# Performance work log

Measured on AMD Instinct MI355X. Metric: run time of the kernel, lower is better.

## Reference

```python
import jax, jax.numpy as jnp
import numpy as np

B, IN, H, D, C, K = 4096, 128, 256, 32, 8, 256
HS = D // 2  # structure_filter hidden (latent_dim > 2)
EPS = 1e-6
MAX_NORM = 0.99


def _gelu(t):
    return jax.nn.gelu(t, approximate=False)  # torch nn.GELU default = exact erf


def _project_to_ball(z):
    norm = jnp.maximum(jnp.linalg.norm(z, axis=-1, keepdims=True), EPS)
    scale = jnp.minimum(MAX_NORM / norm, 1.0)
    return z * scale


def _hyperbolic_distance(xp, yp):
    # Poincare-ball distance: arccosh(1 + 2*|x-y|^2 / ((1-|x|^2)(1-|y|^2)))
    sq = jnp.sum((xp - yp) ** 2, axis=-1)
    xn = jnp.sum(xp * xp, axis=-1)
    yn = jnp.sum(yp * yp, axis=-1)
    denom = jnp.maximum((1.0 - xn) * (1.0 - yn), EPS)
    arg = jnp.maximum(1.0 + 2.0 * sq / denom, 1.0 + EPS)
    return jnp.arccosh(arg)


def setup_inputs() -> dict:
    key = jax.random.key(0)
    ks = jax.random.split(key, 14)
    n = lambda k, shape, s: (jax.random.normal(k, shape, dtype=jnp.float32) * s)
    centers = jax.random.normal(ks[7], (C, D), dtype=jnp.float32)
    centers = centers / jnp.maximum(jnp.linalg.norm(centers, axis=-1, keepdims=True), EPS)
    return {
        "x": jax.random.normal(ks[0], (B, IN), dtype=jnp.float32),
        "W1": n(ks[1], (IN, H), 0.05), "b1": jnp.zeros((H,), jnp.float32),
        "W2": n(ks[2], (H, H), 0.05), "b2": jnp.zeros((H,), jnp.float32),
        "Wv": n(ks[3], (H, D), 0.05), "bv": jnp.zeros((D,), jnp.float32),
        "centers": centers,
        "codebook": n(ks[8], (C, K, D), 0.02),
        "Ws1": n(ks[9], (D, HS), 0.1), "bs1": jnp.zeros((HS,), jnp.float32),
        "Ws2": n(ks[10], (HS, D), 0.1), "bs2": jnp.zeros((D,), jnp.float32),
    }


def reference(x, W1, b1, W2, b2, Wv, bv, centers, codebook, Ws1, bs1, Ws2, bs2):
    sg = jax.lax.stop_gradient
    feats = _gelu(_gelu(x @ W1 + b1) @ W2 + b2)          # [B,H]
    v = feats @ Wv + bv                                   # [B,D]
    scores = (v @ centers.T) / jnp.sqrt(jnp.asarray(D, v.dtype))
    router = jax.nn.softmax(scores, axis=-1)              # [B,C]
    K_chart = jnp.argmax(router, axis=1)                  # [B]
    c_bar = router @ centers                              # [B,D]
    v_local = v - c_bar                                   # [B,D]
    diff = v_local[:, None, None, :] - codebook[None]     # [B,C,K,D]
    dist = jnp.sum(diff * diff, axis=-1)                  # [B,C,K]
    indices = jnp.argmin(dist, axis=-1)                   # [B,C]
    z_q_all = codebook[jnp.arange(C)[None, :], indices]   # [B,C,D]
    v_bc = jnp.broadcast_to(v_local[:, None, :], z_q_all.shape)
    v_proj = _project_to_ball(v_bc)
    w_det = sg(router)
    d_cb = _hyperbolic_distance(z_q_all, sg(v_proj))      # [B,C]
    codebook_loss = jnp.sum(jnp.mean(d_cb ** 2 * w_det, axis=0))
    d_cm = _hyperbolic_distance(sg(z_q_all), v_proj)
    commitment = jnp.sum(jnp.mean(d_cm ** 2 * w_det, axis=0))
    vq_loss = codebook_loss + 0.25 * commitment
    z_q_blended = jnp.sum(z_q_all * router[..., None], axis=1)  # [B,D]
    K_code = jnp.take_along_axis(indices, K_chart[:, None], axis=1)[:, 0]
    delta = v_local[:, None, :] - sg(z_q_all)             # [B,C,D]
    z_n_all = _gelu(delta @ Ws1 + bs1) @ Ws2 + bs2        # [B,C,D]
    z_n = jnp.sum(z_n_all * router[..., None], axis=1)    # [B,D]
    z_tex = (v_local - sg(z_q_blended)) - z_n
    z_q_st = v_local + sg(z_q_blended - v_local)
    z_geo = c_bar + z_q_st + z_n
    return (K_chart, K_code, z_n, z_tex, router, z_geo, vq_loss, indices, z_n_all, c_bar, v_local)
```

## Files before the change

### kernel.cpp

```cpp
#include <hip/hip_runtime.h>
#include <math.h>

#define NB 4096
#define NIN 128
#define NH 256
#define ND 32
#define NC 8
#define NK 256
#define NHS 16

#define OFF_KCHART 0
#define OFF_KCODE  4096
#define OFF_ZN     8192
#define OFF_ZTEX   (OFF_ZN + 4096*32)
#define OFF_ROUTER (OFF_ZTEX + 4096*32)
#define OFF_ZGEO   (OFF_ROUTER + 4096*8)
#define OFF_LOSS   (OFF_ZGEO + 4096*32)
#define OFF_IND    (OFF_LOSS + 1)
#define OFF_ZNALL  (OFF_IND + 4096*8)
#define OFF_CBAR   (OFF_ZNALL + 4096*8*32)
#define OFF_VLOC   (OFF_CBAR + 4096*32)

__device__ __forceinline__ float gelu_exact(float x) {
    return x * (erff(x / 1.41421356237309504f) + 1.0f) * 0.5f;
}

template<int K>
__global__ __launch_bounds__(256)
void gemm_bias_gelu(const float* __restrict__ A, const float* __restrict__ W,
                    const float* __restrict__ bias, float* __restrict__ out) {
    const int N = 256;
    __shared__ float sB[2][32][68];
    const int t  = threadIdx.x;
    const int n0 = blockIdx.x * 64;
    const int r0 = blockIdx.y * 64;
    const int ty = t >> 4, tx = t & 15;
    const int bk = t >> 4, bc = t & 15;

    float4 bias4 = *(const float4*)(bias + n0 + tx * 4);

    float4 pb0 = *(const float4*)(W + bk * N + n0 + bc * 4);
    float4 pb1 = *(const float4*)(W + (bk + 16) * N + n0 + bc * 4);

    const float* Ab0 = A + (r0 + ty * 4 + 0) * K;
    const float* Ab1 = A + (r0 + ty * 4 + 1) * K;
    const float* Ab2 = A + (r0 + ty * 4 + 2) * K;
    const float* Ab3 = A + (r0 + ty * 4 + 3) * K;
    float ac[4][4], an[4][4];
    {
        float4 c0 = *(const float4*)(Ab0 + 0), c1 = *(const float4*)(Ab1 + 0);
        float4 c2 = *(const float4*)(Ab2 + 0), c3 = *(const float4*)(Ab3 + 0);
        ac[0][0]=c0.x; ac[0][1]=c0.y; ac[0][2]=c0.z; ac[0][3]=c0.w;
        ac[1][0]=c1.x; ac[1][1]=c1.y; ac[1][2]=c1.z; ac[1][3]=c1.w;
        ac[2][0]=c2.x; ac[2][1]=c2.y; ac[2][2]=c2.z; ac[2][3]=c2.w;
        ac[3][0]=c3.x; ac[3][1]=c3.y; ac[3][2]=c3.z; ac[3][3]=c3.w;
        float4 n0v = *(const float4*)(Ab0 + 4), n1v = *(const float4*)(Ab1 + 4);
        float4 n2v = *(const float4*)(Ab2 + 4), n3v = *(const float4*)(Ab3 + 4);
        an[0][0]=n0v.x; an[0][1]=n0v.y; an[0][2]=n0v.z; an[0][3]=n0v.w;
        an[1][0]=n1v.x; an[1][1]=n1v.y; an[1][2]=n1v.z; an[1][3]=n1v.w;
        an[2][0]=n2v.x; an[2][1]=n2v.y; an[2][2]=n2v.z; an[2][3]=n2v.w;
        an[3][0]=n3v.x; an[3][1]=n3v.y; an[3][2]=n3v.z; an[3][3]=n3v.w;
    }

    float acc[4][4];
    #pragma unroll
    for (int i = 0; i < 4; i++)
        #pragma unroll
        for (int j = 0; j < 4; j++) acc[i][j] = 0.f;

    int buf = 0;
    for (int kk = 0; kk < K; kk += 32) {
        *(float4*)(&sB[buf][bk][bc*4])    = pb0;
        *(float4*)(&sB[buf][bk+16][bc*4]) = pb1;
        __syncthreads();
        if (kk + 32 < K) {
            pb0 = *(const float4*)(W + (kk + 32 + bk) * N + n0 + bc * 4);
            pb1 = *(const float4*)(W + (kk + 32 + bk + 16) * N + n0 + bc * 4);
        }
        #pragma unroll
        for (int c = 0; c < 8; c++) {
            int knext = kk + (c + 2) * 4;
            if (knext > K - 4) knext = K - 4;
            float4 p0 = *(const float4*)(Ab0 + knext);
            float4 p1 = *(const float4*)(Ab1 + knext);
            float4 p2 = *(const float4*)(Ab2 + knext);
            float4 p3 = *(const float4*)(Ab3 + knext);
            #pragma unroll
            for (int u = 0; u < 4; u++) {
                float4 bv = *(const float4*)(&sB[buf][c * 4 + u][tx * 4]);
                float bb[4] = {bv.x, bv.y, bv.z, bv.w};
                #pragma unroll
                for (int j = 0; j < 4; j++) {
                    acc[0][j] = fmaf(ac[0][u], bb[j], acc[0][j]);
                    acc[1][j] = fmaf(ac[1][u], bb[j], acc[1][j]);
                    acc[2][j] = fmaf(ac[2][u], bb[j], acc[2][j]);
                    acc[3][j] = fmaf(ac[3][u], bb[j], acc[3][j]);
                }
            }
            #pragma unroll
            for (int u = 0; u < 4; u++) {
                ac[0][u] = an[0][u]; ac[1][u] = an[1][u];
                ac[2][u] = an[2][u]; ac[3][u] = an[3][u];
            }
            an[0][0]=p0.x; an[0][1]=p0.y; an[0][2]=p0.z; an[0][3]=p0.w;
            an[1][0]=p1.x; an[1][1]=p1.y; an[1][2]=p1.z; an[1][3]=p1.w;
            an[2][0]=p2.x; an[2][1]=p2.y; an[2][2]=p2.z; an[2][3]=p2.w;
            an[3][0]=p3.x; an[3][1]=p3.y; an[3][2]=p3.z; an[3][3]=p3.w;
        }
        buf ^= 1;
    }
    float bb4[4] = {bias4.x, bias4.y, bias4.z, bias4.w};
    #pragma unroll
    for (int i = 0; i < 4; i++) {
        int row = r0 + ty * 4 + i;
        float4 o;
        float* op = (float*)&o;
        #pragma unroll
        for (int j = 0; j < 4; j++) op[j] = gelu_exact(acc[i][j] + bb4[j]);
        *(float4*)(out + row * N + n0 + tx * 4) = o;
    }
}

__global__ __launch_bounds__(256)
void router_kernel(const float* __restrict__ feats, const float* __restrict__ Wv,
                   const float* __restrict__ bv, const float* __restrict__ centers,
                   float* __restrict__ out, float* __restrict__ vloc_ws) {
    __shared__ float sWvT[ND][260];
    __shared__ float sCent[NC * ND];
    __shared__ float sV[16][ND + 1];
    __shared__ float sRout[16][NC];
    const int t = threadIdx.x;
    {
        #pragma unroll
        for (int q = 0; q < 8; q++) {
            int id = t + q * 256;
            int k = id >> 3, c4 = (id & 7) * 4;
            float4 w = ((const float4*)Wv)[id];
            sWvT[c4 + 0][k] = w.x;
            sWvT[c4 + 1][k] = w.y;
            sWvT[c4 + 2][k] = w.z;
            sWvT[c4 + 3][k] = w.w;
        }
        if (t < 64) ((float4*)sCent)[t] = ((const float4*)centers)[t];
    }
    __syncthreads();
    const int r = t >> 4, cp = t & 15;
    const int row = blockIdx.x * 16 + r;
    float a0 = bv[cp], a1 = bv[cp + 16];
    const float4* f4 = (const float4*)(feats + row * NH);
    for (int k4 = 0; k4 < NH / 4; k4++) {
        float4 f = f4[k4];
        float4 w0 = *(const float4*)(&sWvT[cp][k4 * 4]);
        float4 w1 = *(const float4*)(&sWvT[cp + 16][k4 * 4]);
        a0 = fmaf(f.x, w0.x, a0); a1 = fmaf(f.x, w1.x, a1);
        a0 = fmaf(f.y, w0.y, a0); a1 = fmaf(f.y, w1.y, a1);
        a0 = fmaf(f.z, w0.z, a0); a1 = fmaf(f.z, w1.z, a1);
        a0 = fmaf(f.w, w0.w, a0); a1 = fmaf(f.w, w1.w, a1);
    }
    sV[r][cp] = a0; sV[r][cp + 16] = a1;
    __syncthreads();
    if (t < 16) {
        const int rr = t, grow = blockIdx.x * 16 + rr;
        float sc[NC];
        float m = -3.4e38f; int kmax = 0;
        #pragma unroll
        for (int c = 0; c < NC; c++) {
            float acc = 0.f;
            #pragma unroll
            for (int k = 0; k < ND; k++) acc = fmaf(sV[rr][k], sCent[c * ND + k], acc);
            acc = acc / 5.65685424949238f;
            sc[c] = acc;
            if (acc > m) { m = acc; kmax = c; }
        }
        float s = 0.f;
        #pragma unroll
        for (int c = 0; c < NC; c++) { float e = expf(sc[c] - m); sc[c] = e; s += e; }
        float inv = 1.f / s;
        #pragma unroll
        for (int c = 0; c < NC; c++) {
            float rv = sc[c] * inv;
            sRout[rr][c] = rv;
            out[OFF_ROUTER + grow * NC + c] = rv;
        }
        out[OFF_KCHART + grow] = (float)kmax;
    }
    __syncthreads();
    #pragma unroll
    for (int j = 0; j < 2; j++) {
        int col = cp + j * 16;
        float cb = 0.f;
        #pragma unroll
        for (int c = 0; c < NC; c++) cb = fmaf(sRout[r][c], sCent[c * ND + col], cb);
        float vl = sV[r][col] - cb;
        out[OFF_CBAR + row * ND + col] = cb;
        out[OFF_VLOC + row * ND + col] = vl;
        vloc_ws[row * ND + col] = vl;
    }
}

__global__ __launch_bounds__(256)
void vq_chart(const float* __restrict__ codebook, const float* __restrict__ vloc_ws,
              const float* __restrict__ Ws1, const float* __restrict__ bs1,
              const float* __restrict__ Ws2, const float* __restrict__ bs2,
              float* __restrict__ out, float* __restrict__ loss_partial) {
    __shared__ float sCB[NK][36];
    __shared__ float sV[64][36];
    __shared__ float sBest[8][64];
    __shared__ int   sBidx[8][64];
    __shared__ int   sSel[64];
    __shared__ float sRoutv[64];
    __shared__ float sPscale[64];
    __shared__ float sLossArr[64];
    __shared__ float sWs1[ND][17];
    __shared__ float sWs2[NHS][33];
    __shared__ float sbs1[NHS], sbs2v[ND];
    const int t = threadIdx.x;
    const int c = blockIdx.x & 7;
    const int row0 = (blockIdx.x >> 3) * 64;

    {
        const float4* src = (const float4*)(codebook + c * NK * ND);
        #pragma unroll
        for (int q = 0; q < 8; q++) {
            int id = t + q * 256;
            int code = id >> 3, kq = (id & 7) * 4;
            *(float4*)(&sCB[code][kq]) = src[id];
        }
        #pragma unroll
        for (int q = 0; q < 2; q++) {
            int id = t + q * 256;
            int rr = id >> 3, kq = (id & 7) * 4;
            *(float4*)(&sV[rr][kq]) = ((const float4*)(vloc_ws + row0 * ND))[id];
        }
    }
    if (t < 128) {
        float4 w = ((const float4*)Ws1)[t];
        int k = t >> 2, o = (t & 3) * 4;
        sWs1[k][o] = w.x; sWs1[k][o+1] = w.y; sWs1[k][o+2] = w.z; sWs1[k][o+3] = w.w;
    } else {
        int u = t - 128;
        float4 w = ((const float4*)Ws2)[u];
        int k = u >> 3, o = (u & 7) * 4;
        sWs2[k][o] = w.x; sWs2[k][o+1] = w.y; sWs2[k][o+2] = w.z; sWs2[k][o+3] = w.w;
    }
    if (t < NHS) sbs1[t] = bs1[t];
    else if (t < NHS + ND) sbs2v[t - NHS] = bs2[t - NHS];
    if (t < 64) sRoutv[t] = out[OFF_ROUTER + (row0 + t) * NC + c];
    __syncthreads();

    const int r = t & 31, g = t >> 5;
    float vl0[ND], vl1[ND];
    #pragma unroll
    for (int q = 0; q < 8; q++) {
        float4 a = *(const float4*)(&sV[r][q * 4]);
        vl0[q*4] = a.x; vl0[q*4+1] = a.y; vl0[q*4+2] = a.z; vl0[q*4+3] = a.w;
        float4 b = *(const float4*)(&sV[r + 32][q * 4]);
        vl1[q*4] = b.x; vl1[q*4+1] = b.y; vl1[q*4+2] = b.z; vl1[q*4+3] = b.w;
    }
    float best0 = 3.4e38f, best1 = 3.4e38f;
    int bi0 = 0, bi1 = 0;
    for (int j = 0; j < 32; j++) {
        const int code = g * 32 + j;
        float dot0 = 0.f, dot1 = 0.f, en2 = 0.f;
        #pragma unroll
        for (int q = 0; q < 8; q++) {
            float4 e = *(const float4*)(&sCB[code][q * 4]);
            en2  = fmaf(e.x, e.x, en2);
            dot0 = fmaf(vl0[q*4+0], e.x, dot0); dot1 = fmaf(vl1[q*4+0], e.x, dot1);
            en2  = fmaf(e.y, e.y, en2);
            dot0 = fmaf(vl0[q*4+1], e.y, dot0); dot1 = fmaf(vl1[q*4+1], e.y, dot1);
            en2  = fmaf(e.z, e.z, en2);
            dot0 = fmaf(vl0[q*4+2], e.z, dot0); dot1 = fmaf(vl1[q*4+2], e.z, dot1);
            en2  = fmaf(e.w, e.w, en2);
            dot0 = fmaf(vl0[q*4+3], e.w, dot0); dot1 = fmaf(vl1[q*4+3], e.w, dot1);
        }
        float d0 = en2 - 2.f * dot0;
        float d1 = en2 - 2.f * dot1;
        if (d0 < best0) { best0 = d0; bi0 = code; }
        if (d1 < best1) { best1 = d1; bi1 = code; }
    }
    sBest[g][r] = best0;      sBidx[g][r] = bi0;
    sBest[g][r + 32] = best1; sBidx[g][r + 32] = bi1;
    __syncthreads();
    if (t < 64) {
        float bb = sBest[0][t]; int ii = sBidx[0][t];
        #pragma unroll
        for (int gg = 1; gg < 8; gg++) {
            float v = sBest[gg][t];
            if (v < bb) { bb = v; ii = sBidx[gg][t]; }
        }
        sSel[t] = ii;
        out[OFF_IND + (row0 + t) * NC + c] = (float)ii;
        float vn2 = 0.f;
        #pragma unroll
        for (int k = 0; k < ND; k++) { float v = sV[t][k]; vn2 = fmaf(v, v, vn2); }
        float norm = fmaxf(sqrtf(vn2), 1e-6f);
        sPscale[t] = fminf(0.99f / norm, 1.0f);
    }
    __syncthreads();

    const int i = t & 15, r16 = t >> 4;
    const float b1r = sbs1[i];
    const float bo0 = sbs2v[2*i], bo1 = sbs2v[2*i+1];
    #pragma unroll
    for (int pass = 0; pass < 4; pass++) {
        const int lrow = pass * 16 + r16;
        const int grow = row0 + lrow;
        const int sel = sSel[lrow];
        const float rc = sRoutv[lrow];
        const float ps = sPscale[lrow];
        float acc1 = b1r;
        #pragma unroll
        for (int k = 0; k < ND; k++) {
            float dlt = sV[lrow][k] - sCB[sel][k];
            acc1 = fmaf(dlt, sWs1[k][i], acc1);
        }
        float h = gelu_exact(acc1);
        float a0 = bo0, a1 = bo1;
        #pragma unroll
        for (int k = 0; k < NHS; k++) {
            float s1k = __shfl(h, k, 16);
            a0 = fmaf(s1k, sWs2[k][2*i],   a0);
            a1 = fmaf(s1k, sWs2[k][2*i+1], a1);
        }
        out[OFF_ZNALL + (grow * NC + c) * ND + 2*i]     = a0;
        out[OFF_ZNALL + (grow * NC + c) * ND + 2*i + 1] = a1;
        const float e0 = sCB[sel][2*i], e1 = sCB[sel][2*i+1];
        float yp0 = sV[lrow][2*i] * ps, yp1 = sV[lrow][2*i+1] * ps;
        float d0 = e0 - yp0, d1 = e1 - yp1;
        float sq = fmaf(d0, d0, d1 * d1);
        float xn = fmaf(e0, e0, e1 * e1);
        float yn = fmaf(yp0, yp0, yp1 * yp1);
        #pragma unroll
        for (int m = 1; m < 16; m <<= 1) {
            sq += __shfl_xor(sq, m, 16);
            xn += __shfl_xor(xn, m, 16);
            yn += __shfl_xor(yn, m, 16);
        }
        if (i == 0) {
            float denom = fmaxf((1.f - xn) * (1.f - yn), 1e-6f);
            float arg = fmaxf(1.f + 2.f * sq / denom, 1.f + 1e-6f);
            float dd = acoshf(arg);
            sLossArr[lrow] = dd * dd * rc;
        }
    }
    __syncthreads();
    if (t < 64) {
        float v = sLossArr[t];
        #pragma unroll
        for (int off = 32; off > 0; off >>= 1) v += __shfl_down(v, off, 64);
        if (t == 0) loss_partial[blockIdx.x] = v;
    }
}

__global__ __launch_bounds__(256)
void finalize2_kernel(const float* __restrict__ codebook, const float* __restrict__ vloc_ws,
                      float* __restrict__ out, const float* __restrict__ partials) {
    const int gid = blockIdx.x * 256 + threadIdx.x;
    const int row = gid >> 4;
    const int cp = gid & 15;
    float rout[NC]; int ind[NC];
    #pragma unroll
    for (int cc = 0; cc < NC; cc++) {
        rout[cc] = out[OFF_ROUTER + row * NC + cc];
        ind[cc]  = (int)out[OFF_IND + row * NC + cc];
    }
    float zn0 = 0.f, zn1 = 0.f, zq0 = 0.f, zq1 = 0.f;
    #pragma unroll
    for (int cc = 0; cc < NC; cc++) {
        const float rcc = rout[cc];
        zn0 = fmaf(out[OFF_ZNALL + (row * NC + cc) * ND + 2*cp],     rcc, zn0);
        zn1 = fmaf(out[OFF_ZNALL + (row * NC + cc) * ND + 2*cp + 1], rcc, zn1);
        const float* e = codebook + (cc * NK + ind[cc]) * ND + 2*cp;
        zq0 = fmaf(e[0], rcc, zq0);
        zq1 = fmaf(e[1], rcc, zq1);
    }
    const float v0 = vloc_ws[row * ND + 2*cp], v1 = vloc_ws[row * ND + 2*cp + 1];
    const float cb0 = out[OFF_CBAR + row * ND + 2*cp];
    const float cb1 = out[OFF_CBAR + row * ND + 2*cp + 1];
    out[OFF_ZN   + row * ND + 2*cp]     = zn0;
    out[OFF_ZN   + row * ND + 2*cp + 1] = zn1;
    out[OFF_ZTEX + row * ND + 2*cp]     = v0 - zq0 - zn0;
    out[OFF_ZTEX + row * ND + 2*cp + 1] = v1 - zq1 - zn1;
    out[OFF_ZGEO + row * ND + 2*cp]     = cb0 + zq0 + zn0;
    out[OFF_ZGEO + row * ND + 2*cp + 1] = cb1 + zq1 + zn1;
    if (cp == 0) {
        int kc = (int)out[OFF_KCHART + row];
        out[OFF_KCODE + row] = out[OFF_IND + row * NC + kc];
    }
    if (blockIdx.x == 0) {
        __shared__ float sTmp[4];
        const int t = threadIdx.x;
        float v = partials[t] + partials[t + 256];
        #pragma unroll
        for (int off = 32; off > 0; off >>= 1) v += __shfl_down(v, off, 64);
        if ((t & 63) == 0) sTmp[t >> 6] = v;
        __syncthreads();
        if (t == 0) out[OFF_LOSS] = 1.25f * (sTmp[0] + sTmp[1] + sTmp[2] + sTmp[3]) / 4096.f;
    }
}

extern "C" void kernel_launch(void* const* d_in, const int* in_sizes, int n_in,
                              void* d_out, int out_size, void* d_ws, size_t ws_size,
                              hipStream_t stream) {
    const float* x        = (const float*)d_in[0];
    const float* W1       = (const float*)d_in[1];
    const float* b1       = (const float*)d_in[2];
    const float* W2       = (const float*)d_in[3];
    const float* b2       = (const float*)d_in[4];
    const float* Wv       = (const float*)d_in[5];
    const float* bv       = (const float*)d_in[6];
    const float* centers  = (const float*)d_in[7];
    const float* codebook = (const float*)d_in[8];
    const float* Ws1      = (const float*)d_in[9];
    const float* bs1      = (const float*)d_in[10];
    const float* Ws2      = (const float*)d_in[11];
    const float* bs2      = (const float*)d_in[12];
    float* out = (float*)d_out;
    float* ws  = (float*)d_ws;

    float* h1       = ws;
    float* feats    = ws + 4096 * 256;
    float* vloc     = ws + 2 * 4096 * 256;
    float* partials = ws + 2 * 4096 * 256 + 4096 * 32;

    gemm_bias_gelu<128><<<dim3(4, 64), dim3(256), 0, stream>>>(x, W1, b1, h1);
    gemm_bias_gelu<256><<<dim3(4, 64), dim3(256), 0, stream>>>(h1, W2, b2, feats);
    router_kernel<<<dim3(256), dim3(256), 0, stream>>>(feats, Wv, bv, centers, out, vloc);
    vq_chart<<<dim3(512), dim3(256), 0, stream>>>(codebook, vloc, Ws1, bs1, Ws2, bs2, out, partials);
    finalize2_kernel<<<dim3(256), dim3(256), 0, stream>>>(codebook, vloc, out, partials);
}
```

Baseline: 69.60 us.

## Halve per-block row tiles to double grid sizes and precompute codebook norms

The two GEMM kernels now give each thread 2 rows instead of 4, so the row tile per block drops from 64 to 32 and the grid doubles to 512 blocks. The router kernel handles 8 rows per block with one output column per thread, and spreads the center scores over 64 threads. Finalize uses one column per thread with twice the blocks. The VQ kernel computes codebook squared norms once into shared memory instead of inside the distance loop. More blocks should fill the 256 CUs better, at the cost of less register reuse per thread in the GEMMs and more redundant weight and codebook staging per block.

```diff
diff --git a/kernel.cpp b/kernel.cpp
--- a/kernel.cpp
+++ b/kernel.cpp
@@ -33,7 +33,7 @@
     __shared__ float sB[2][32][68];
     const int t  = threadIdx.x;
     const int n0 = blockIdx.x * 64;
-    const int r0 = blockIdx.y * 64;
+    const int r0 = blockIdx.y * 32;
     const int ty = t >> 4, tx = t & 15;
     const int bk = t >> 4, bc = t & 15;
 
@@ -42,29 +42,21 @@
     float4 pb0 = *(const float4*)(W + bk * N + n0 + bc * 4);
     float4 pb1 = *(const float4*)(W + (bk + 16) * N + n0 + bc * 4);
 
-    const float* Ab0 = A + (r0 + ty * 4 + 0) * K;
-    const float* Ab1 = A + (r0 + ty * 4 + 1) * K;
-    const float* Ab2 = A + (r0 + ty * 4 + 2) * K;
-    const float* Ab3 = A + (r0 + ty * 4 + 3) * K;
-    float ac[4][4], an[4][4];
+    const float* Ab0 = A + (r0 + ty * 2 + 0) * K;
+    const float* Ab1 = A + (r0 + ty * 2 + 1) * K;
+    float ac[2][4], an[2][4];
     {
         float4 c0 = *(const float4*)(Ab0 + 0), c1 = *(const float4*)(Ab1 + 0);
-        float4 c2 = *(const float4*)(Ab2 + 0), c3 = *(const float4*)(Ab3 + 0);
         ac[0][0]=c0.x; ac[0][1]=c0.y; ac[0][2]=c0.z; ac[0][3]=c0.w;
         ac[1][0]=c1.x; ac[1][1]=c1.y; ac[1][2]=c1.z; ac[1][3]=c1.w;
-        ac[2][0]=c2.x; ac[2][1]=c2.y; ac[2][2]=c2.z; ac[2][3]=c2.w;
-        ac[3][0]=c3.x; ac[3][1]=c3.y; ac[3][2]=c3.z; ac[3][3]=c3.w;
-        float4 n0v = *(const float4*)(Ab0 + 4), n1v = *(const float4*)(Ab1 + 4);
-        float4 n2v = *(const float4*)(Ab2 + 4), n3v = *(const float4*)(Ab3 + 4);
-        an[0][0]=n0v.x; an[0][1]=n0v.y; an[0][2]=n0v.z; an[0][3]=n0v.w;
-        an[1][0]=n1v.x; an[1][1]=n1v.y; an[1][2]=n1v.z; an[1][3]=n1v.w;
-        an[2][0]=n2v.x; an[2][1]=n2v.y; an[2][2]=n2v.z; an[2][3]=n2v.w;
-        an[3][0]=n3v.x; an[3][1]=n3v.y; an[3][2]=n3v.z; an[3][3]=n3v.w;
-    }
-
-    float acc[4][4];
-    #pragma unroll
-    for (int i = 0; i < 4; i++)
+        float4 d0 = *(const float4*)(Ab0 + 4), d1 = *(const float4*)(Ab1 + 4);
+        an[0][0]=d0.x; an[0][1]=d0.y; an[0][2]=d0.z; an[0][3]=d0.w;
+        an[1][0]=d1.x; an[1][1]=d1.y; an[1][2]=d1.z; an[1][3]=d1.w;
+    }
+
+    float acc[2][4];
+    #pragma unroll
+    for (int i = 0; i < 2; i++)
         #pragma unroll
         for (int j = 0; j < 4; j++) acc[i][j] = 0.f;
 
@@ -83,8 +75,6 @@
             if (knext > K - 4) knext = K - 4;
             float4 p0 = *(const float4*)(Ab0 + knext);
             float4 p1 = *(const float4*)(Ab1 + knext);
-            float4 p2 = *(const float4*)(Ab2 + knext);
-            float4 p3 = *(const float4*)(Ab3 + knext);
             #pragma unroll
             for (int u = 0; u < 4; u++) {
                 float4 bv = *(const float4*)(&sB[buf][c * 4 + u][tx * 4]);
@@ -93,26 +83,19 @@
                 for (int j = 0; j < 4; j++) {
                     acc[0][j] = fmaf(ac[0][u], bb[j], acc[0][j]);
                     acc[1][j] = fmaf(ac[1][u], bb[j], acc[1][j]);
-                    acc[2][j] = fmaf(ac[2][u], bb[j], acc[2][j]);
-                    acc[3][j] = fmaf(ac[3][u], bb[j], acc[3][j]);
                 }
             }
             #pragma unroll
-            for (int u = 0; u < 4; u++) {
-                ac[0][u] = an[0][u]; ac[1][u] = an[1][u];
-                ac[2][u] = an[2][u]; ac[3][u] = an[3][u];
-            }
+            for (int u = 0; u < 4; u++) { ac[0][u] = an[0][u]; ac[1][u] = an[1][u]; }
             an[0][0]=p0.x; an[0][1]=p0.y; an[0][2]=p0.z; an[0][3]=p0.w;
             an[1][0]=p1.x; an[1][1]=p1.y; an[1][2]=p1.z; an[1][3]=p1.w;
-            an[2][0]=p2.x; an[2][1]=p2.y; an[2][2]=p2.z; an[2][3]=p2.w;
-            an[3][0]=p3.x; an[3][1]=p3.y; an[3][2]=p3.z; an[3][3]=p3.w;
         }
         buf ^= 1;
     }
     float bb4[4] = {bias4.x, bias4.y, bias4.z, bias4.w};
     #pragma unroll
-    for (int i = 0; i < 4; i++) {
-        int row = r0 + ty * 4 + i;
+    for (int i = 0; i < 2; i++) {
+        int row = r0 + ty * 2 + i;
         float4 o;
         float* op = (float*)&o;
         #pragma unroll
@@ -127,9 +110,11 @@
                    float* __restrict__ out, float* __restrict__ vloc_ws) {
     __shared__ float sWvT[ND][260];
     __shared__ float sCent[NC * ND];
-    __shared__ float sV[16][ND + 1];
-    __shared__ float sRout[16][NC];
+    __shared__ float sV[8][ND + 2];
+    __shared__ float sScore[8][NC];
+    __shared__ float sRout[8][NC];
     const int t = threadIdx.x;
+    const int row0 = blockIdx.x * 8;
     {
         #pragma unroll
         for (int q = 0; q < 8; q++) {
@@ -144,38 +129,42 @@
         if (t < 64) ((float4*)sCent)[t] = ((const float4*)centers)[t];
     }
     __syncthreads();
-    const int r = t >> 4, cp = t & 15;
-    const int row = blockIdx.x * 16 + r;
-    float a0 = bv[cp], a1 = bv[cp + 16];
+    const int r = t >> 5, cp = t & 31;
+    const int row = row0 + r;
+    float a0 = bv[cp];
     const float4* f4 = (const float4*)(feats + row * NH);
     for (int k4 = 0; k4 < NH / 4; k4++) {
         float4 f = f4[k4];
-        float4 w0 = *(const float4*)(&sWvT[cp][k4 * 4]);
-        float4 w1 = *(const float4*)(&sWvT[cp + 16][k4 * 4]);
-        a0 = fmaf(f.x, w0.x, a0); a1 = fmaf(f.x, w1.x, a1);
-        a0 = fmaf(f.y, w0.y, a0); a1 = fmaf(f.y, w1.y, a1);
-        a0 = fmaf(f.z, w0.z, a0); a1 = fmaf(f.z, w1.z, a1);
-        a0 = fmaf(f.w, w0.w, a0); a1 = fmaf(f.w, w1.w, a1);
-    }
-    sV[r][cp] = a0; sV[r][cp + 16] = a1;
-    __syncthreads();
-    if (t < 16) {
-        const int rr = t, grow = blockIdx.x * 16 + rr;
+        float4 w = *(const float4*)(&sWvT[cp][k4 * 4]);
+        a0 = fmaf(f.x, w.x, a0);
+        a0 = fmaf(f.y, w.y, a0);
+        a0 = fmaf(f.z, w.z, a0);
+        a0 = fmaf(f.w, w.w, a0);
+    }
+    sV[r][cp] = a0;
+    __syncthreads();
+    if (t < 64) {
+        int rr = t >> 3, c = t & 7;
+        float s = 0.f;
+        #pragma unroll
+        for (int k = 0; k < ND; k++) s = fmaf(sV[rr][k], sCent[c * ND + k], s);
+        sScore[rr][c] = s / 5.65685424949238f;
+    }
+    __syncthreads();
+    if (t < 8) {
+        const int rr = t, grow = row0 + rr;
         float sc[NC];
         float m = -3.4e38f; int kmax = 0;
         #pragma unroll
         for (int c = 0; c < NC; c++) {
-            float acc = 0.f;
-            #pragma unroll
-            for (int k = 0; k < ND; k++) acc = fmaf(sV[rr][k], sCent[c * ND + k], acc);
-            acc = acc / 5.65685424949238f;
-            sc[c] = acc;
-            if (acc > m) { m = acc; kmax = c; }
-        }
-        float s = 0.f;
-        #pragma unroll
-        for (int c = 0; c < NC; c++) { float e = expf(sc[c] - m); sc[c] = e; s += e; }
-        float inv = 1.f / s;
+            float s = sScore[rr][c];
+            sc[c] = s;
+            if (s > m) { m = s; kmax = c; }
+        }
+        float ssum = 0.f;
+        #pragma unroll
+        for (int c = 0; c < NC; c++) { float e = expf(sc[c] - m); sc[c] = e; ssum += e; }
+        float inv = 1.f / ssum;
         #pragma unroll
         for (int c = 0; c < NC; c++) {
             float rv = sc[c] * inv;
@@ -185,9 +174,8 @@
         out[OFF_KCHART + grow] = (float)kmax;
     }
     __syncthreads();
-    #pragma unroll
-    for (int j = 0; j < 2; j++) {
-        int col = cp + j * 16;
+    {
+        const int col = cp;
         float cb = 0.f;
         #pragma unroll
         for (int c = 0; c < NC; c++) cb = fmaf(sRout[r][c], sCent[c * ND + col], cb);
@@ -204,6 +192,7 @@
               const float* __restrict__ Ws2, const float* __restrict__ bs2,
               float* __restrict__ out, float* __restrict__ loss_partial) {
     __shared__ float sCB[NK][36];
+    __shared__ float sEn2[NK];
     __shared__ float sV[64][36];
     __shared__ float sBest[8][64];
     __shared__ int   sBidx[8][64];
@@ -247,6 +236,17 @@
     else if (t < NHS + ND) sbs2v[t - NHS] = bs2[t - NHS];
     if (t < 64) sRoutv[t] = out[OFF_ROUTER + (row0 + t) * NC + c];
     __syncthreads();
+    {
+        float s = 0.f;
+        #pragma unroll
+        for (int q = 0; q < 8; q++) {
+            float4 e = *(const float4*)(&sCB[t][q * 4]);
+            s = fmaf(e.x, e.x, s); s = fmaf(e.y, e.y, s);
+            s = fmaf(e.z, e.z, s); s = fmaf(e.w, e.w, s);
+        }
+        sEn2[t] = s;
+    }
+    __syncthreads();
 
     const int r = t & 31, g = t >> 5;
     float vl0[ND], vl1[ND];
@@ -261,19 +261,16 @@
     int bi0 = 0, bi1 = 0;
     for (int j = 0; j < 32; j++) {
         const int code = g * 32 + j;
-        float dot0 = 0.f, dot1 = 0.f, en2 = 0.f;
+        float dot0 = 0.f, dot1 = 0.f;
         #pragma unroll
         for (int q = 0; q < 8; q++) {
             float4 e = *(const float4*)(&sCB[code][q * 4]);
-            en2  = fmaf(e.x, e.x, en2);
             dot0 = fmaf(vl0[q*4+0], e.x, dot0); dot1 = fmaf(vl1[q*4+0], e.x, dot1);
-            en2  = fmaf(e.y, e.y, en2);
             dot0 = fmaf(vl0[q*4+1], e.y, dot0); dot1 = fmaf(vl1[q*4+1], e.y, dot1);
-            en2  = fmaf(e.z, e.z, en2);
             dot0 = fmaf(vl0[q*4+2], e.z, dot0); dot1 = fmaf(vl1[q*4+2], e.z, dot1);
-            en2  = fmaf(e.w, e.w, en2);
             dot0 = fmaf(vl0[q*4+3], e.w, dot0); dot1 = fmaf(vl1[q*4+3], e.w, dot1);
         }
+        const float en2 = sEn2[code];
         float d0 = en2 - 2.f * dot0;
         float d1 = en2 - 2.f * dot1;
         if (d0 < best0) { best0 = d0; bi0 = code; }
@@ -357,34 +354,27 @@
 void finalize2_kernel(const float* __restrict__ codebook, const float* __restrict__ vloc_ws,
                       float* __restrict__ out, const float* __restrict__ partials) {
     const int gid = blockIdx.x * 256 + threadIdx.x;
-    const int row = gid >> 4;
-    const int cp = gid & 15;
+    const int row = gid >> 5;
+    const int col = gid & 31;
     float rout[NC]; int ind[NC];
     #pragma unroll
     for (int cc = 0; cc < NC; cc++) {
         rout[cc] = out[OFF_ROUTER + row * NC + cc];
         ind[cc]  = (int)out[OFF_IND + row * NC + cc];
     }
-    float zn0 = 0.f, zn1 = 0.f, zq0 = 0.f, zq1 = 0.f;
+    float zn = 0.f, zq = 0.f;
     #pragma unroll
     for (int cc = 0; cc < NC; cc++) {
         const float rcc = rout[cc];
-        zn0 = fmaf(out[OFF_ZNALL + (row * NC + cc) * ND + 2*cp],     rcc, zn0);
-        zn1 = fmaf(out[OFF_ZNALL + (row * NC + cc) * ND + 2*cp + 1], rcc, zn1);
-        const float* e = codebook + (cc * NK + ind[cc]) * ND + 2*cp;
-        zq0 = fmaf(e[0], rcc, zq0);
-        zq1 = fmaf(e[1], rcc, zq1);
-    }
-    const float v0 = vloc_ws[row * ND + 2*cp], v1 = vloc_ws[row * ND + 2*cp + 1];
-    const float cb0 = out[OFF_CBAR + row * ND + 2*cp];
-    const float cb1 = out[OFF_CBAR + row * ND + 2*cp + 1];
-    out[OFF_ZN   + row * ND + 2*cp]     = zn0;
-    out[OFF_ZN   + row * ND + 2*cp + 1] = zn1;
-    out[OFF_ZTEX + row * ND + 2*cp]     = v0 - zq0 - zn0;
-    out[OFF_ZTEX + row * ND + 2*cp + 1] = v1 - zq1 - zn1;
-    out[OFF_ZGEO + row * ND + 2*cp]     = cb0 + zq0 + zn0;
-    out[OFF_ZGEO + row * ND + 2*cp + 1] = cb1 + zq1 + zn1;
-    if (cp == 0) {
+        zn = fmaf(out[OFF_ZNALL + (row * NC + cc) * ND + col], rcc, zn);
+        zq = fmaf(codebook[(cc * NK + ind[cc]) * ND + col], rcc, zq);
+    }
+    const float vl = vloc_ws[row * ND + col];
+    const float cb = out[OFF_CBAR + row * ND + col];
+    out[OFF_ZN   + row * ND + col] = zn;
+    out[OFF_ZTEX + row * ND + col] = vl - zq - zn;
+    out[OFF_ZGEO + row * ND + col] = cb + zq + zn;
+    if (col == 0) {
         int kc = (int)out[OFF_KCHART + row];
         out[OFF_KCODE + row] = out[OFF_IND + row * NC + kc];
     }
@@ -424,9 +414,9 @@
     float* vloc     = ws + 2 * 4096 * 256;
     float* partials = ws + 2 * 4096 * 256 + 4096 * 32;
 
-    gemm_bias_gelu<128><<<dim3(4, 64), dim3(256), 0, stream>>>(x, W1, b1, h1);
-    gemm_bias_gelu<256><<<dim3(4, 64), dim3(256), 0, stream>>>(h1, W2, b2, feats);
-    router_kernel<<<dim3(256), dim3(256), 0, stream>>>(feats, Wv, bv, centers, out, vloc);
+    gemm_bias_gelu<128><<<dim3(4, 128), dim3(256), 0, stream>>>(x, W1, b1, h1);
+    gemm_bias_gelu<256><<<dim3(4, 128), dim3(256), 0, stream>>>(h1, W2, b2, feats);
+    router_kernel<<<dim3(512), dim3(256), 0, stream>>>(feats, Wv, bv, centers, out, vloc);
     vq_chart<<<dim3(512), dim3(256), 0, stream>>>(codebook, vloc, Ws1, bs1, Ws2, bs2, out, partials);
-    finalize2_kernel<<<dim3(256), dim3(256), 0, stream>>>(codebook, vloc, out, partials);
-}
+    finalize2_kernel<<<dim3(512), dim3(256), 0, stream>>>(codebook, vloc, out, partials);
+}
```

Result: faster. 59.96 us (-13.9%).
